# Performance work log

Hardware: AMD Instinct MI355X
Metric: run time of the kernel (lower is better)

Reference implementation:

```python
import jax, jax.numpy as jnp
import numpy as np

N_NODES = 100000
N_EDGES = 3200000
D_IN, D_HID, D_OUT = 128, 16, 2


def gcn_conv(x, src, dst, W, b, n_nodes):
    """PyG GCNConv: D^-1/2 (A+I) D^-1/2 X W + b (self-loops added, sym norm)."""
    h = x @ W  # [N, d_out] - transform before aggregation (small d_out)
    # add self loops
    loop = jnp.arange(n_nodes, dtype=src.dtype)
    src2 = jnp.concatenate([src, loop])
    dst2 = jnp.concatenate([dst, loop])
    # degree (in-degree incl. self loop) and symmetric normalization
    deg = jax.ops.segment_sum(jnp.ones_like(dst2, dtype=h.dtype), dst2,
                              num_segments=n_nodes)
    dinv = jax.lax.rsqrt(deg)  # deg >= 1 due to self loops
    norm = dinv[src2] * dinv[dst2]  # [E+N]
    msg = h[src2] * norm[:, None]   # gather + scale
    out = jax.ops.segment_sum(msg, dst2, num_segments=n_nodes)  # scatter-add
    return out + b


def setup_inputs() -> dict:
    key = jax.random.key(0)
    k1, k2, k3, k4, k5, k6 = jax.random.split(key, 6)
    x = jax.random.normal(k1, (N_NODES, D_IN), dtype=jnp.float32)
    edge_index = jax.random.randint(k2, (2, N_EDGES), 0, N_NODES, dtype=jnp.int64)
    # Glorot-style init for GCNConv weights, zero bias (PyG default)
    W1 = jax.random.normal(k3, (D_IN, D_HID), dtype=jnp.float32) / np.sqrt(D_IN)
    b1 = jnp.zeros((D_HID,), dtype=jnp.float32)
    W2 = jax.random.normal(k4, (D_HID, D_OUT), dtype=jnp.float32) / np.sqrt(D_HID)
    b2 = jnp.zeros((D_OUT,), dtype=jnp.float32)
    return {"x": x, "W1": W1, "b1": b1, "W2": W2, "b2": b2,
            "edge_index": edge_index}


def reference(x, W1, b1, W2, b2, edge_index):
    src, dst = edge_index[0], edge_index[1]
    h = jax.nn.relu(gcn_conv(x, src, dst, W1, b1, N_NODES))
    h = gcn_conv(h, src, dst, W2, b2, N_NODES)
    return jax.nn.log_softmax(h, axis=1)
```

## Files before the change

### kernel.cpp

```cpp
#include <hip/hip_runtime.h>

#define NN 100000
#define NE 3200000
#define DIN 128
#define DHID 16
#define DOUT 2
#define NBUCK 391
#define EPT 16
#define BHT 1024
#define EPB (BHT * EPT)
#define NBB ((NE + EPB - 1) / EPB)

__device__ __forceinline__ unsigned f2bf(float f) {
    unsigned u = __float_as_uint(f);
    return (u + 0x7FFFu + ((u >> 16) & 1u)) >> 16;
}
__device__ __forceinline__ float bflo(unsigned a) { return __uint_as_float(a << 16); }
__device__ __forceinline__ float bfhi(unsigned a) { return __uint_as_float(a & 0xFFFF0000u); }

__global__ __launch_bounds__(512) void k_zero_b(int* __restrict__ bcount) {
    int t = threadIdx.x;
    if (t < NBUCK) bcount[t] = 0;
}

__global__ __launch_bounds__(BHT) void k_bhist(const int* __restrict__ dst,
                                               int* __restrict__ bcount) {
    __shared__ int h[NBUCK];
    int t = threadIdx.x;
    for (int i = t; i < NBUCK; i += BHT) h[i] = 0;
    __syncthreads();
    long long base = (long long)blockIdx.x * EPB;
#pragma unroll
    for (int k = 0; k < EPT; ++k) {
        long long e = base + (long long)k * BHT + t;
        if (e < NE) atomicAdd(&h[((unsigned)dst[e]) >> 8], 1);
    }
    __syncthreads();
    for (int i = t; i < NBUCK; i += BHT) {
        int c = h[i];
        if (c) atomicAdd(&bcount[i], c);
    }
}

__global__ __launch_bounds__(512) void k_bscan(const int* __restrict__ bcount,
                                               int* __restrict__ bstart,
                                               int* __restrict__ bcursor) {
    __shared__ int sc[512];
    int t = threadIdx.x;
    int c = (t < NBUCK) ? bcount[t] : 0;
    sc[t] = c;
    __syncthreads();
    for (int off = 1; off < 512; off <<= 1) {
        int v = sc[t];
        int add = (t >= off) ? sc[t - off] : 0;
        __syncthreads();
        sc[t] = v + add;
        __syncthreads();
    }
    int excl = sc[t] - c;
    if (t <= NBUCK) bstart[t] = excl;
    if (t < NBUCK) bcursor[t] = excl;
}

__global__ __launch_bounds__(BHT) void k_bfill(const int* __restrict__ src,
                                               const int* __restrict__ dst,
                                               int* __restrict__ bcursor,
                                               unsigned* __restrict__ packed) {
    __shared__ int h[NBUCK];
    __shared__ int hbase[NBUCK];
    int t = threadIdx.x;
    for (int i = t; i < NBUCK; i += BHT) h[i] = 0;
    __syncthreads();
    long long base = (long long)blockIdx.x * EPB;
    int ed[EPT], es[EPT];
#pragma unroll
    for (int k = 0; k < EPT; ++k) {
        long long e = base + (long long)k * BHT + t;
        if (e < NE) {
            ed[k] = dst[e];
            es[k] = src[e];
            atomicAdd(&h[((unsigned)ed[k]) >> 8], 1);
        } else {
            ed[k] = -1;
            es[k] = 0;
        }
    }
    __syncthreads();
    for (int i = t; i < NBUCK; i += BHT) {
        int c = h[i];
        hbase[i] = c ? atomicAdd(&bcursor[i], c) : 0;
    }
    __syncthreads();
    for (int i = t; i < NBUCK; i += BHT) h[i] = 0;
    __syncthreads();
#pragma unroll
    for (int k = 0; k < EPT; ++k) {
        if (ed[k] >= 0) {
            unsigned d = (unsigned)ed[k];
            int b = d >> 8;
            int off = atomicAdd(&h[b], 1);
            packed[hbase[b] + off] = ((d & 255u) << 24) | (unsigned)es[k];
        }
    }
}

__global__ __launch_bounds__(256) void k_pass2(const int* __restrict__ bstart,
                                               const unsigned* __restrict__ packed,
                                               int* __restrict__ rowstart,
                                               float* __restrict__ dinv,
                                               int* __restrict__ esrc) {
    __shared__ int h[256], sc[256], cur[256];
    int b = blockIdx.x;
    int t = threadIdx.x;
    int dst0 = b << 8;
    int ebeg = bstart[b];
    int eend = bstart[b + 1];
    h[t] = 0;
    __syncthreads();
    for (int p = ebeg + t; p < eend; p += 256)
        atomicAdd(&h[packed[p] >> 24], 1);
    __syncthreads();
    int c = h[t];
    sc[t] = c;
    __syncthreads();
    for (int off = 1; off < 256; off <<= 1) {
        int v = sc[t];
        int add = (t >= off) ? sc[t - off] : 0;
        __syncthreads();
        sc[t] = v + add;
        __syncthreads();
    }
    int gpos = ebeg + sc[t] - c;
    int v = dst0 + t;
    if (v < NN) {
        rowstart[v] = gpos;
        dinv[v] = rsqrtf((float)(c + 1));
    }
    cur[t] = gpos;
    if (b == 0 && t == 0) rowstart[NN] = NE;
    __syncthreads();
    for (int p = ebeg + t; p < eend; p += 256) {
        unsigned pk = packed[p];
        int pos = atomicAdd(&cur[pk >> 24], 1);
        esrc[pos] = (int)(pk & 0xFFFFFFu);
    }
}

__global__ __launch_bounds__(256) void k_mm1(const float* __restrict__ x,
                                             const float* __restrict__ W1,
                                             const float* __restrict__ dinv,
                                             unsigned* __restrict__ g1b) {
    __shared__ float Ws[DIN * DHID];
    for (int i = threadIdx.x; i < DIN * DHID; i += 256) Ws[i] = W1[i];
    __syncthreads();
    int t = blockIdx.x * 256 + threadIdx.x;
    int v = t >> 2;
    int q = threadIdx.x & 3;
    if (v >= NN) return;
    float4 xq[8];
    const float4* xr = (const float4*)(x + (size_t)v * DIN + q * 32);
#pragma unroll
    for (int i = 0; i < 8; ++i) xq[i] = xr[i];
    const float* xs = (const float*)xq;
    float acc0 = 0.f, acc1 = 0.f, acc2 = 0.f, acc3 = 0.f;
#define QSTEP(QQ, CTRL)                                                          \
    _Pragma("unroll")                                                            \
    for (int k = 0; k < 32; ++k) {                                               \
        float xv = __int_as_float(                                               \
            __builtin_amdgcn_mov_dpp(__float_as_int(xs[k]), CTRL, 0xF, 0xF, false)); \
        const float4 w = *(const float4*)&Ws[(QQ * 32 + k) * DHID + q * 4];      \
        acc0 += xv * w.x; acc1 += xv * w.y; acc2 += xv * w.z; acc3 += xv * w.w;  \
    }
    QSTEP(0, 0x00)
    QSTEP(1, 0x55)
    QSTEP(2, 0xAA)
    QSTEP(3, 0xFF)
#undef QSTEP
    float dv = dinv[v];
    unsigned u0 = f2bf(acc0 * dv) | (f2bf(acc1 * dv) << 16);
    unsigned u1 = f2bf(acc2 * dv) | (f2bf(acc3 * dv) << 16);
    ((uint2*)(g1b + (size_t)v * 8))[q] = make_uint2(u0, u1);
}

__global__ __launch_bounds__(256) void k_gather1mm2(const int* __restrict__ rowstart,
                                                    const int* __restrict__ esrc,
                                                    const float* __restrict__ dinv,
                                                    const unsigned* __restrict__ G,
                                                    const float* __restrict__ b1,
                                                    const float* __restrict__ W2,
                                                    float* __restrict__ g2) {
    int t = blockIdx.x * 256 + threadIdx.x;
    int v = t >> 3;
    int j = t & 7;
    if (v >= NN) return;
    int beg = rowstart[v];
    int end = rowstart[v + 1];
    unsigned a = G[(v << 3) + j];
    float c0 = bflo(a), c1 = bfhi(a);
    int p = beg;
    int n4 = beg + ((end - beg) & ~3);
    for (; p < n4; p += 4) {
        int u0 = esrc[p], u1 = esrc[p + 1], u2 = esrc[p + 2], u3 = esrc[p + 3];
        unsigned b0 = G[(u0 << 3) + j];
        unsigned b1w = G[(u1 << 3) + j];
        unsigned b2w = G[(u2 << 3) + j];
        unsigned b3w = G[(u3 << 3) + j];
        c0 += bflo(b0) + bflo(b1w) + bflo(b2w) + bflo(b3w);
        c1 += bfhi(b0) + bfhi(b1w) + bfhi(b2w) + bfhi(b3w);
    }
    for (; p < end; ++p) {
        unsigned b = G[(esrc[p] << 3) + j];
        c0 += bflo(b);
        c1 += bfhi(b);
    }
    float dv = dinv[v];
    float o0 = fmaxf(c0 * dv + b1[2 * j], 0.f);
    float o1 = fmaxf(c1 * dv + b1[2 * j + 1], 0.f);
    float p0 = o0 * W2[(2 * j) * 2 + 0] + o1 * W2[(2 * j + 1) * 2 + 0];
    float p1 = o0 * W2[(2 * j) * 2 + 1] + o1 * W2[(2 * j + 1) * 2 + 1];
    p0 += __shfl_xor(p0, 1); p0 += __shfl_xor(p0, 2); p0 += __shfl_xor(p0, 4);
    p1 += __shfl_xor(p1, 1); p1 += __shfl_xor(p1, 2); p1 += __shfl_xor(p1, 4);
    if (j == 0) {
        float2 w = make_float2(p0 * dv, p1 * dv);
        *(float2*)(g2 + (size_t)v * 2) = w;
    }
}

__global__ __launch_bounds__(256) void k_gather2(const int* __restrict__ rowstart,
                                                 const int* __restrict__ esrc,
                                                 const float* __restrict__ dinv,
                                                 const float* __restrict__ g2,
                                                 const float* __restrict__ b2,
                                                 float* __restrict__ out) {
    int t = blockIdx.x * 256 + threadIdx.x;
    int v = t >> 3;
    if (v >= NN) return;
    int lane = t & 7;
    int ch = lane & 1;
    int slot = lane >> 1;
    int beg = rowstart[v];
    int end = rowstart[v + 1];
    float acc = 0.0f;
    for (int p = beg + slot; p < end; p += 4)
        acc += g2[(esrc[p] << 1) + ch];
    acc += __shfl_xor(acc, 2);
    acc += __shfl_xor(acc, 4);
    float o = (acc + g2[(v << 1) + ch]) * dinv[v] + b2[ch];
    float other = __shfl_xor(o, 1);
    float m = fmaxf(o, other);
    float lse = m + logf(expf(o - m) + expf(other - m));
    if (slot == 0) out[(v << 1) + ch] = o - lse;
}

extern "C" void kernel_launch(void* const* d_in, const int* in_sizes, int n_in,
                              void* d_out, int out_size, void* d_ws, size_t ws_size,
                              hipStream_t stream) {
    const float* x  = (const float*)d_in[0];
    const float* W1 = (const float*)d_in[1];
    const float* b1 = (const float*)d_in[2];
    const float* W2 = (const float*)d_in[3];
    const float* b2 = (const float*)d_in[4];
    const int* ei   = (const int*)d_in[5];
    const int* src = ei;
    const int* dst = ei + NE;

    int* ws       = (int*)d_ws;
    int* bcount   = ws;
    int* bstart   = ws + 400;
    int* bcursor  = ws + 800;
    int* rowstart = ws + 1200;
    float* dinv   = (float*)(ws + 1200 + NN + 16);
    int* esrc     = ws + 1200 + 2 * NN + 16;
    unsigned* packed = (unsigned*)(esrc + NE);
    unsigned* g1b = packed;
    float* g2     = (float*)(packed + NE);

    float* out = (float*)d_out;

    k_zero_b<<<1, 512, 0, stream>>>(bcount);
    k_bhist<<<NBB, BHT, 0, stream>>>(dst, bcount);
    k_bscan<<<1, 512, 0, stream>>>(bcount, bstart, bcursor);
    k_bfill<<<NBB, BHT, 0, stream>>>(src, dst, bcursor, packed);
    k_pass2<<<NBUCK, 256, 0, stream>>>(bstart, packed, rowstart, dinv, esrc);
    k_mm1<<<(NN * 4 + 255) / 256, 256, 0, stream>>>(x, W1, dinv, g1b);
    k_gather1mm2<<<(NN * 8 + 255) / 256, 256, 0, stream>>>(rowstart, esrc, dinv, g1b, b1, W2, g2);
    k_gather2<<<(NN * 8 + 255) / 256, 256, 0, stream>>>(rowstart, esrc, dinv, g2, b2, out);
}
```

Baseline: 140.0 us.

## Aggregate per-bucket in shared memory with LDS atomics instead of building CSR

```diff
diff --git a/kernel.cpp b/kernel.cpp
--- a/kernel.cpp
+++ b/kernel.cpp
@@ -10,6 +10,7 @@
 #define BHT 1024
 #define EPB (BHT * EPT)
 #define NBB ((NE + EPB - 1) / EPB)
+#define GTH 512
 
 __device__ __forceinline__ unsigned f2bf(float f) {
     unsigned u = __float_as_uint(f);
@@ -104,46 +105,20 @@
     }
 }
 
-__global__ __launch_bounds__(256) void k_pass2(const int* __restrict__ bstart,
+__global__ __launch_bounds__(GTH) void k_dinvb(const int* __restrict__ bstart,
                                                const unsigned* __restrict__ packed,
-                                               int* __restrict__ rowstart,
-                                               float* __restrict__ dinv,
-                                               int* __restrict__ esrc) {
-    __shared__ int h[256], sc[256], cur[256];
+                                               float* __restrict__ dinv) {
+    __shared__ int h[256];
     int b = blockIdx.x;
     int t = threadIdx.x;
-    int dst0 = b << 8;
-    int ebeg = bstart[b];
-    int eend = bstart[b + 1];
-    h[t] = 0;
-    __syncthreads();
-    for (int p = ebeg + t; p < eend; p += 256)
-        atomicAdd(&h[packed[p] >> 24], 1);
-    __syncthreads();
-    int c = h[t];
-    sc[t] = c;
-    __syncthreads();
-    for (int off = 1; off < 256; off <<= 1) {
-        int v = sc[t];
-        int add = (t >= off) ? sc[t - off] : 0;
-        __syncthreads();
-        sc[t] = v + add;
-        __syncthreads();
-    }
-    int gpos = ebeg + sc[t] - c;
-    int v = dst0 + t;
-    if (v < NN) {
-        rowstart[v] = gpos;
-        dinv[v] = rsqrtf((float)(c + 1));
-    }
-    cur[t] = gpos;
-    if (b == 0 && t == 0) rowstart[NN] = NE;
-    __syncthreads();
-    for (int p = ebeg + t; p < eend; p += 256) {
-        unsigned pk = packed[p];
-        int pos = atomicAdd(&cur[pk >> 24], 1);
-        esrc[pos] = (int)(pk & 0xFFFFFFu);
-    }
+    if (t < 256) h[t] = 0;
+    __syncthreads();
+    int ebeg = bstart[b], eend = bstart[b + 1];
+    for (int e = ebeg + t; e < eend; e += GTH)
+        atomicAdd(&h[packed[e] >> 24], 1);
+    __syncthreads();
+    int v = (b << 8) + t;
+    if (t < 256 && v < NN) dinv[v] = rsqrtf((float)(h[t] + 1));
 }
 
 __global__ __launch_bounds__(256) void k_mm1(const float* __restrict__ x,
@@ -182,74 +157,126 @@
     ((uint2*)(g1b + (size_t)v * 8))[q] = make_uint2(u0, u1);
 }
 
-__global__ __launch_bounds__(256) void k_gather1mm2(const int* __restrict__ rowstart,
-                                                    const int* __restrict__ esrc,
-                                                    const float* __restrict__ dinv,
-                                                    const unsigned* __restrict__ G,
-                                                    const float* __restrict__ b1,
-                                                    const float* __restrict__ W2,
-                                                    float* __restrict__ g2) {
-    int t = blockIdx.x * 256 + threadIdx.x;
-    int v = t >> 3;
-    int j = t & 7;
-    if (v >= NN) return;
-    int beg = rowstart[v];
-    int end = rowstart[v + 1];
-    unsigned a = G[(v << 3) + j];
-    float c0 = bflo(a), c1 = bfhi(a);
-    int p = beg;
-    int n4 = beg + ((end - beg) & ~3);
-    for (; p < n4; p += 4) {
-        int u0 = esrc[p], u1 = esrc[p + 1], u2 = esrc[p + 2], u3 = esrc[p + 3];
-        unsigned b0 = G[(u0 << 3) + j];
-        unsigned b1w = G[(u1 << 3) + j];
-        unsigned b2w = G[(u2 << 3) + j];
-        unsigned b3w = G[(u3 << 3) + j];
-        c0 += bflo(b0) + bflo(b1w) + bflo(b2w) + bflo(b3w);
-        c1 += bfhi(b0) + bfhi(b1w) + bfhi(b2w) + bfhi(b3w);
-    }
-    for (; p < end; ++p) {
-        unsigned b = G[(esrc[p] << 3) + j];
-        c0 += bflo(b);
-        c1 += bfhi(b);
-    }
-    float dv = dinv[v];
-    float o0 = fmaxf(c0 * dv + b1[2 * j], 0.f);
-    float o1 = fmaxf(c1 * dv + b1[2 * j + 1], 0.f);
-    float p0 = o0 * W2[(2 * j) * 2 + 0] + o1 * W2[(2 * j + 1) * 2 + 0];
-    float p1 = o0 * W2[(2 * j) * 2 + 1] + o1 * W2[(2 * j + 1) * 2 + 1];
-    p0 += __shfl_xor(p0, 1); p0 += __shfl_xor(p0, 2); p0 += __shfl_xor(p0, 4);
-    p1 += __shfl_xor(p1, 1); p1 += __shfl_xor(p1, 2); p1 += __shfl_xor(p1, 4);
-    if (j == 0) {
-        float2 w = make_float2(p0 * dv, p1 * dv);
-        *(float2*)(g2 + (size_t)v * 2) = w;
-    }
-}
-
-__global__ __launch_bounds__(256) void k_gather2(const int* __restrict__ rowstart,
-                                                 const int* __restrict__ esrc,
-                                                 const float* __restrict__ dinv,
-                                                 const float* __restrict__ g2,
-                                                 const float* __restrict__ b2,
-                                                 float* __restrict__ out) {
-    int t = blockIdx.x * 256 + threadIdx.x;
-    int v = t >> 3;
-    if (v >= NN) return;
-    int lane = t & 7;
-    int ch = lane & 1;
-    int slot = lane >> 1;
-    int beg = rowstart[v];
-    int end = rowstart[v + 1];
-    float acc = 0.0f;
-    for (int p = beg + slot; p < end; p += 4)
-        acc += g2[(esrc[p] << 1) + ch];
-    acc += __shfl_xor(acc, 2);
-    acc += __shfl_xor(acc, 4);
-    float o = (acc + g2[(v << 1) + ch]) * dinv[v] + b2[ch];
-    float other = __shfl_xor(o, 1);
-    float m = fmaxf(o, other);
-    float lse = m + logf(expf(o - m) + expf(other - m));
-    if (slot == 0) out[(v << 1) + ch] = o - lse;
+__global__ __launch_bounds__(GTH) void k_gth1(const int* __restrict__ bstart,
+                                              const unsigned* __restrict__ packed,
+                                              const float* __restrict__ dinv,
+                                              const unsigned* __restrict__ G,
+                                              const float* __restrict__ b1,
+                                              const float* __restrict__ W2,
+                                              float* __restrict__ g2) {
+    __shared__ float acc[256][17];
+    int b = blockIdx.x;
+    int t = threadIdx.x;
+    int v0 = b << 8;
+    if (t < 256) {
+        int v = v0 + t;
+        if (v < NN) {
+            const uint4* gp = (const uint4*)(G + ((size_t)v << 3));
+            uint4 ga = gp[0], gb = gp[1];
+            acc[t][0] = bflo(ga.x);  acc[t][1] = bfhi(ga.x);
+            acc[t][2] = bflo(ga.y);  acc[t][3] = bfhi(ga.y);
+            acc[t][4] = bflo(ga.z);  acc[t][5] = bfhi(ga.z);
+            acc[t][6] = bflo(ga.w);  acc[t][7] = bfhi(ga.w);
+            acc[t][8] = bflo(gb.x);  acc[t][9] = bfhi(gb.x);
+            acc[t][10] = bflo(gb.y); acc[t][11] = bfhi(gb.y);
+            acc[t][12] = bflo(gb.z); acc[t][13] = bfhi(gb.z);
+            acc[t][14] = bflo(gb.w); acc[t][15] = bfhi(gb.w);
+        } else {
+#pragma unroll
+            for (int ch = 0; ch < 16; ++ch) acc[t][ch] = 0.f;
+        }
+    }
+    __syncthreads();
+    int ebeg = bstart[b], eend = bstart[b + 1];
+    int slot = t >> 3, j = t & 7;
+    int e = ebeg + slot;
+    for (; e + 64 < eend; e += 128) {
+        unsigned pk0 = packed[e];
+        unsigned pk1 = packed[e + 64];
+        unsigned ga = G[((size_t)(pk0 & 0xFFFFFFu) << 3) + j];
+        unsigned gb = G[((size_t)(pk1 & 0xFFFFFFu) << 3) + j];
+        int d0 = pk0 >> 24;
+        int d1 = pk1 >> 24;
+        atomicAdd(&acc[d0][2 * j], bflo(ga));
+        atomicAdd(&acc[d0][2 * j + 1], bfhi(ga));
+        atomicAdd(&acc[d1][2 * j], bflo(gb));
+        atomicAdd(&acc[d1][2 * j + 1], bfhi(gb));
+    }
+    if (e < eend) {
+        unsigned pk0 = packed[e];
+        unsigned ga = G[((size_t)(pk0 & 0xFFFFFFu) << 3) + j];
+        int d0 = pk0 >> 24;
+        atomicAdd(&acc[d0][2 * j], bflo(ga));
+        atomicAdd(&acc[d0][2 * j + 1], bfhi(ga));
+    }
+    __syncthreads();
+    if (t < 256) {
+        int v = v0 + t;
+        if (v < NN) {
+            float dv = dinv[v];
+            float p0 = 0.f, p1 = 0.f;
+#pragma unroll
+            for (int ch = 0; ch < 16; ++ch) {
+                float o = fmaxf(acc[t][ch] * dv + b1[ch], 0.f);
+                p0 = fmaf(o, W2[ch * 2 + 0], p0);
+                p1 = fmaf(o, W2[ch * 2 + 1], p1);
+            }
+            *(float2*)(g2 + (size_t)v * 2) = make_float2(p0 * dv, p1 * dv);
+        }
+    }
+}
+
+__global__ __launch_bounds__(GTH) void k_gth2(const int* __restrict__ bstart,
+                                              const unsigned* __restrict__ packed,
+                                              const float* __restrict__ dinv,
+                                              const float* __restrict__ g2,
+                                              const float* __restrict__ b2,
+                                              float* __restrict__ out) {
+    __shared__ float acc2[256][3];
+    int b = blockIdx.x;
+    int t = threadIdx.x;
+    int v0 = b << 8;
+    if (t < 256) {
+        int v = v0 + t;
+        float2 s = (v < NN) ? *(const float2*)(g2 + (size_t)v * 2)
+                            : make_float2(0.f, 0.f);
+        acc2[t][0] = s.x;
+        acc2[t][1] = s.y;
+    }
+    __syncthreads();
+    int ebeg = bstart[b], eend = bstart[b + 1];
+    int e = ebeg + t;
+    for (; e + GTH < eend; e += 2 * GTH) {
+        unsigned pk0 = packed[e];
+        unsigned pk1 = packed[e + GTH];
+        float2 s0 = *(const float2*)(g2 + ((size_t)(pk0 & 0xFFFFFFu) << 1));
+        float2 s1 = *(const float2*)(g2 + ((size_t)(pk1 & 0xFFFFFFu) << 1));
+        int d0 = pk0 >> 24;
+        int d1 = pk1 >> 24;
+        atomicAdd(&acc2[d0][0], s0.x);
+        atomicAdd(&acc2[d0][1], s0.y);
+        atomicAdd(&acc2[d1][0], s1.x);
+        atomicAdd(&acc2[d1][1], s1.y);
+    }
+    if (e < eend) {
+        unsigned pk0 = packed[e];
+        float2 s0 = *(const float2*)(g2 + ((size_t)(pk0 & 0xFFFFFFu) << 1));
+        int d0 = pk0 >> 24;
+        atomicAdd(&acc2[d0][0], s0.x);
+        atomicAdd(&acc2[d0][1], s0.y);
+    }
+    __syncthreads();
+    if (t < 256) {
+        int v = v0 + t;
+        if (v < NN) {
+            float dv = dinv[v];
+            float a0 = acc2[t][0] * dv + b2[0];
+            float a1 = acc2[t][1] * dv + b2[1];
+            float m = fmaxf(a0, a1);
+            float lse = m + logf(expf(a0 - m) + expf(a1 - m));
+            *(float2*)(out + (size_t)v * 2) = make_float2(a0 - lse, a1 - lse);
+        }
+    }
 }
 
 extern "C" void kernel_launch(void* const* d_in, const int* in_sizes, int n_in,
@@ -268,12 +295,10 @@
     int* bcount   = ws;
     int* bstart   = ws + 400;
     int* bcursor  = ws + 800;
-    int* rowstart = ws + 1200;
-    float* dinv   = (float*)(ws + 1200 + NN + 16);
-    int* esrc     = ws + 1200 + 2 * NN + 16;
-    unsigned* packed = (unsigned*)(esrc + NE);
-    unsigned* g1b = packed;
-    float* g2     = (float*)(packed + NE);
+    float* dinv   = (float*)(ws + 1200);
+    unsigned* packed = (unsigned*)(ws + 1200 + NN + 16);
+    unsigned* g1b = packed + NE;
+    float* g2     = (float*)(g1b + 8 * NN);
 
     float* out = (float*)d_out;
 
@@ -281,8 +306,8 @@
     k_bhist<<<NBB, BHT, 0, stream>>>(dst, bcount);
     k_bscan<<<1, 512, 0, stream>>>(bcount, bstart, bcursor);
     k_bfill<<<NBB, BHT, 0, stream>>>(src, dst, bcursor, packed);
-    k_pass2<<<NBUCK, 256, 0, stream>>>(bstart, packed, rowstart, dinv, esrc);
+    k_dinvb<<<NBUCK, GTH, 0, stream>>>(bstart, packed, dinv);
     k_mm1<<<(NN * 4 + 255) / 256, 256, 0, stream>>>(x, W1, dinv, g1b);
-    k_gather1mm2<<<(NN * 8 + 255) / 256, 256, 0, stream>>>(rowstart, esrc, dinv, g1b, b1, W2, g2);
-    k_gather2<<<(NN * 8 + 255) / 256, 256, 0, stream>>>(rowstart, esrc, dinv, g2, b2, out);
-}
+    k_gth1<<<NBUCK, GTH, 0, stream>>>(bstart, packed, dinv, g1b, b1, W2, g2);
+    k_gth2<<<NBUCK, GTH, 0, stream>>>(bstart, packed, dinv, g2, b2, out);
+}
```

Result: slower. 455.9 us (+225.6%).
